# Kernel optimization log

Hardware: AMD Instinct MI355X
Metric: run time of the kernel (lower is better)

The kernel has to match this reference:

```python
import jax, jax.numpy as jnp
import numpy as np

B, IN_DIM, H1, H2, HID, SPEC_H, OUT, E = 16384, 1024, 2048, 2048, 1024, 2048, 1, 8


def setup_inputs() -> dict:
    key = jax.random.key(0)
    ks = jax.random.split(key, 12)

    def lin(k, fan_in, shape):
        # torch nn.Linear default init: U(-1/sqrt(fan_in), 1/sqrt(fan_in))
        bound = 1.0 / np.sqrt(fan_in)
        return jax.random.uniform(k, shape, jnp.float32, -bound, bound)

    return {
        "x": jax.random.normal(ks[0], (B, IN_DIM), jnp.float32),
        "d": jax.random.randint(ks[1], (B,), 0, E, jnp.int64),
        # shared encoder: Linear(IN,H1)+ReLU, Linear(H1,H2)+ReLU, Linear(H2,HID)
        "enc_W0": lin(ks[2], IN_DIM, (IN_DIM, H1)),
        "enc_b0": lin(ks[3], IN_DIM, (H1,)),
        "enc_W1": lin(ks[4], H1, (H1, H2)),
        "enc_b1": lin(ks[5], H1, (H2,)),
        "enc_W2": lin(ks[6], H2, (H2, HID)),
        "enc_b2": lin(ks[7], H2, (HID,)),
        # per-domain heads: Linear(HID,SPEC_H)+ReLU, Linear(SPEC_H,OUT)
        "spec_W1": lin(ks[8], HID, (E, HID, SPEC_H)),
        "spec_b1": lin(ks[9], HID, (E, SPEC_H)),
        "spec_W2": lin(ks[10], SPEC_H, (E, SPEC_H, OUT)),
        "spec_b2": lin(ks[11], SPEC_H, (E, OUT)),
    }


def reference(x, d, enc_W0, enc_b0, enc_W1, enc_b1, enc_W2, enc_b2,
              spec_W1, spec_b1, spec_W2, spec_b2):
    # Shared encoder (dropout is identity in eval mode)
    z = jax.nn.relu(x @ enc_W0 + enc_b0)        # [B, H1]
    z = jax.nn.relu(z @ enc_W1 + enc_b1)        # [B, H2]
    z = z @ enc_W2 + enc_b2                     # [B, HID]

    # Domain-routed heads: compute each expert on the full batch, combine by mask.
    n_experts = spec_W1.shape[0]
    out = jnp.zeros((z.shape[0], spec_W2.shape[-1]), dtype=z.dtype)  # [B, OUT]
    for e in range(n_experts):
        h = jax.nn.relu(z @ spec_W1[e] + spec_b1[e])  # [B, SPEC_H]
        y = h @ spec_W2[e] + spec_b2[e]               # [B, OUT]
        out = out + jnp.where((d == e)[:, None], y, jnp.zeros_like(y))
    return out
```

## Files before the change

### kernel.cpp

```cpp
#include <hip/hip_runtime.h>
#include <hip/hip_bf16.h>
#include <stdint.h>

#define B_SZ   16384
#define IN_DIM 1024
#define H1     2048
#define H2     2048
#define HID    1024
#define SPEC_H 2048
#define NE     8
#define MAX_TILES 136

typedef __bf16 bf16x8 __attribute__((ext_vector_type(8)));
typedef float  f32x4  __attribute__((ext_vector_type(4)));
typedef ushort us8    __attribute__((ext_vector_type(8)));

__device__ __forceinline__ ushort f2bf(float f) {
  uint32_t u = __float_as_uint(f);
  u += 0x7FFF + ((u >> 16) & 1);
  return (ushort)(u >> 16);
}

__device__ __forceinline__ void gl_lds16(const void* g, void* l) {
  __builtin_amdgcn_global_load_lds(
      (const __attribute__((address_space(1))) void*)g,
      (__attribute__((address_space(3))) void*)l, 16, 0, 0);
}


struct TransDesc { const float* src; ushort* dst; int K, N, nx, base; };

struct PrepArgs {
  TransDesc td[4];
  const float* x; ushort* xb;
  const int* d; int* counts; const float* sb2; float* out;
  int castBase;
  int cntBase;
};

__global__ void prep_all(PrepArgs pa) {
  int g = blockIdx.x;
  int t = threadIdx.x;
  if (g >= pa.cntBase) {
    __shared__ int hist[NE];
    if (t < NE) hist[t] = 0;
    __syncthreads();
    int i = (g - pa.cntBase) * 256 + t;
    int e = pa.d[i];
    atomicAdd(&hist[e], 1);
    pa.out[i] = pa.sb2[e];
    __syncthreads();
    if (t < NE) atomicAdd(&pa.counts[t], hist[t]);
    return;
  }
  if (g >= pa.castBase) {
    size_t i = (size_t)(g - pa.castBase) * 4096 + (size_t)t * 16;
    float4 v0 = *(const float4*)(pa.x + i);
    float4 v1 = *(const float4*)(pa.x + i + 4);
    float4 v2 = *(const float4*)(pa.x + i + 8);
    float4 v3 = *(const float4*)(pa.x + i + 12);
    uint32_t p0 = f2bf(v0.x) | ((uint32_t)f2bf(v0.y) << 16);
    uint32_t p1 = f2bf(v0.z) | ((uint32_t)f2bf(v0.w) << 16);
    uint32_t p2 = f2bf(v1.x) | ((uint32_t)f2bf(v1.y) << 16);
    uint32_t p3 = f2bf(v1.z) | ((uint32_t)f2bf(v1.w) << 16);
    uint32_t p4 = f2bf(v2.x) | ((uint32_t)f2bf(v2.y) << 16);
    uint32_t p5 = f2bf(v2.z) | ((uint32_t)f2bf(v2.w) << 16);
    uint32_t p6 = f2bf(v3.x) | ((uint32_t)f2bf(v3.y) << 16);
    uint32_t p7 = f2bf(v3.z) | ((uint32_t)f2bf(v3.w) << 16);
    int4 pkA = {(int)p0, (int)p1, (int)p2, (int)p3};
    int4 pkB = {(int)p4, (int)p5, (int)p6, (int)p7};
    *(int4*)(pa.xb + i) = pkA;
    *(int4*)(pa.xb + i + 8) = pkB;
    return;
  }
  __shared__ float tile[64][65];
  int wsel = 0;
#pragma unroll
  for (int i = 1; i < 4; ++i)
    if (g >= pa.td[i].base) wsel = i;
  TransDesc dd = pa.td[wsel];
  int local = g - dd.base;
  int per = dd.nx * (dd.K >> 6);
  int z = local / per;
  int r = local - z * per;
  int bx = r % dd.nx, by = r / dd.nx;
  int n0 = bx * 64, k0 = by * 64;
  const float* src = dd.src + (size_t)z * dd.K * dd.N;
  ushort* dst = dd.dst + (size_t)z * dd.K * dd.N;
  int lk = t >> 4;
  int ln4 = (t & 15) * 4;
#pragma unroll
  for (int j = 0; j < 4; ++j) {
    int k = lk + j * 16;
    float4 v = *(const float4*)(src + (size_t)(k0 + k) * dd.N + n0 + ln4);
    tile[ln4 + 0][k] = v.x;
    tile[ln4 + 1][k] = v.y;
    tile[ln4 + 2][k] = v.z;
    tile[ln4 + 3][k] = v.w;
  }
  __syncthreads();
  int kc = (t & 7) * 8;
  int nb = t >> 3;
#pragma unroll
  for (int j = 0; j < 2; ++j) {
    int nn = nb + j * 32;
    us8 o;
#pragma unroll
    for (int q = 0; q < 8; ++q) o[q] = f2bf(tile[nn][kc + q]);
    *(us8*)(dst + (size_t)(n0 + nn) * dd.K + k0 + kc) = o;
  }
}


__global__ void build_k(const int* __restrict__ counts, int* __restrict__ catalog,
                        int* __restrict__ poff, int* __restrict__ cursors) {
  if (threadIdx.x == 0) {
    int off = 0;
    for (int e = 0; e < NE; ++e) {
      poff[e] = off * 128;
      int nt = (counts[e] + 127) >> 7;
      for (int i = 0; i < nt; ++i) catalog[off + i] = e;
      off += nt;
      cursors[e] = 0;
    }
    for (int i = off; i < MAX_TILES; ++i) catalog[i] = -1;
  }
}

__global__ void scatter_k(const int* __restrict__ d, const int* __restrict__ poff,
                          int* __restrict__ cursors, int* __restrict__ perm) {
  __shared__ int wcnt[4][NE];
  __shared__ int basee[NE];
  int t = threadIdx.x;
  int i = blockIdx.x * 256 + t;
  int e = d[i];
  int w = t >> 6, lane = t & 63;
  uint64_t mymask = 0;
#pragma unroll
  for (int ee = 0; ee < NE; ++ee) {
    uint64_t mm = __ballot(e == ee);
    if (lane == 0) wcnt[w][ee] = __popcll(mm);
    if (e == ee) mymask = mm;
  }
  int rank = __popcll(mymask & ((1ull << lane) - 1ull));
  __syncthreads();
  if (t < NE) {
    int s = 0;
#pragma unroll
    for (int ww = 0; ww < 4; ++ww) { int c = wcnt[ww][t]; wcnt[ww][t] = s; s += c; }
    basee[t] = atomicAdd(&cursors[t], s);
  }
  __syncthreads();
  int pos = basee[e] + wcnt[w][e] + rank;
  perm[poff[e] + pos] = i;
}


template <int RELU>
__global__ __launch_bounds__(256, 2) void gemm_bias(
    const ushort* __restrict__ A, const ushort* __restrict__ Bt,
    const float* __restrict__ bias, ushort* __restrict__ C,
    int M, int N, int K, int lognx) {
  __shared__ __align__(16) ushort lA[128 * 64];
  __shared__ __align__(16) ushort lB[128 * 64];
  const int t = threadIdx.x;
  const int h = blockIdx.x;
  const int g = h >> 3;
  const int nx = 1 << lognx;
  const int by = (h & 7) + ((g >> lognx) << 3);
  const int bx = g & (nx - 1);
  const int m0 = by * 128, n0 = bx * 128;
  const int w = t >> 6, lane = t & 63;
  const int wm = (w >> 1) * 64, wn = (w & 1) * 64;
  const int q = lane >> 4, rl = lane & 15;

  f32x4 acc[4][4];
#pragma unroll
  for (int mi = 0; mi < 4; ++mi)
#pragma unroll
    for (int ni = 0; ni < 4; ++ni) acc[mi][ni] = 0.0f;

  const int row_s = t >> 3;
  const int pch_s = t & 7;

  for (int k0 = 0; k0 < K; k0 += 64) {
    __syncthreads();
#pragma unroll
    for (int j = 0; j < 4; ++j) {
      int row = j * 32 + row_s;
      int gch = pch_s ^ (row & 7);
      gl_lds16(A + (size_t)(m0 + row) * K + k0 + gch * 8, lA + j * 2048 + w * 512);
      gl_lds16(Bt + (size_t)(n0 + row) * K + k0 + gch * 8, lB + j * 2048 + w * 512);
    }
    __syncthreads();
#pragma unroll
    for (int kk = 0; kk < 2; ++kk) {
      bf16x8 af[4], bfr[4];
#pragma unroll
      for (int i = 0; i < 4; ++i) {
        int pc = (kk * 4 + q) ^ (rl & 7);
        af[i]  = __builtin_bit_cast(bf16x8, *(const int4*)(lA + (wm + i * 16 + rl) * 64 + pc * 8));
        bfr[i] = __builtin_bit_cast(bf16x8, *(const int4*)(lB + (wn + i * 16 + rl) * 64 + pc * 8));
      }
#pragma unroll
      for (int mi = 0; mi < 4; ++mi)
#pragma unroll
        for (int ni = 0; ni < 4; ++ni)
          acc[mi][ni] = __builtin_amdgcn_mfma_f32_16x16x32_bf16(af[mi], bfr[ni], acc[mi][ni], 0, 0, 0);
    }
  }

  float bv[4];
#pragma unroll
  for (int ni = 0; ni < 4; ++ni) bv[ni] = bias[n0 + wn + ni * 16 + rl];
#pragma unroll
  for (int mi = 0; mi < 4; ++mi) {
    int rg = m0 + wm + mi * 16 + q * 4;
#pragma unroll
    for (int r = 0; r < 4; ++r) {
#pragma unroll
      for (int ni = 0; ni < 4; ++ni) {
        float v = acc[mi][ni][r] + bv[ni];
        if (RELU) v = fmaxf(v, 0.0f);
        C[(size_t)(rg + r) * N + n0 + wn + ni * 16 + rl] = f2bf(v);
      }
    }
  }
}


template <int RELU>
__global__ __launch_bounds__(256, 2) void gemm_bias_256(
    const ushort* __restrict__ A, const ushort* __restrict__ Bt,
    const float* __restrict__ bias, ushort* __restrict__ C,
    int M, int N, int K, int lognx) {
  __shared__ __align__(16) ushort lA[256 * 64];
  __shared__ __align__(16) ushort lB[128 * 64];
  const int t = threadIdx.x;
  const int h = blockIdx.x;
  const int g = h >> 3;
  const int nx = 1 << lognx;
  const int by = (h & 7) + ((g >> lognx) << 3);
  const int bx = g & (nx - 1);
  const int m0 = by * 256, n0 = bx * 128;
  const int w = t >> 6, lane = t & 63;
  const int wm = (w >> 1) * 128, wn = (w & 1) * 64;
  const int q = lane >> 4, rl = lane & 15;

  f32x4 acc[8][4];
#pragma unroll
  for (int mi = 0; mi < 8; ++mi)
#pragma unroll
    for (int ni = 0; ni < 4; ++ni) acc[mi][ni] = 0.0f;

  const int row_s = t >> 3;
  const int pch_s = t & 7;

  for (int k0 = 0; k0 < K; k0 += 64) {
    __syncthreads();
#pragma unroll
    for (int j = 0; j < 8; ++j) {
      int row = j * 32 + row_s;
      int gch = pch_s ^ (row & 7);
      gl_lds16(A + (size_t)(m0 + row) * K + k0 + gch * 8, lA + j * 2048 + w * 512);
    }
#pragma unroll
    for (int j = 0; j < 4; ++j) {
      int row = j * 32 + row_s;
      int gch = pch_s ^ (row & 7);
      gl_lds16(Bt + (size_t)(n0 + row) * K + k0 + gch * 8, lB + j * 2048 + w * 512);
    }
    __syncthreads();
#pragma unroll
    for (int kk = 0; kk < 2; ++kk) {
      bf16x8 bfr[4];
#pragma unroll
      for (int i = 0; i < 4; ++i) {
        int pc = (kk * 4 + q) ^ (rl & 7);
        bfr[i] = __builtin_bit_cast(bf16x8, *(const int4*)(lB + (wn + i * 16 + rl) * 64 + pc * 8));
      }
#pragma unroll
      for (int mi = 0; mi < 8; ++mi) {
        int pc = (kk * 4 + q) ^ (rl & 7);
        bf16x8 af = __builtin_bit_cast(bf16x8, *(const int4*)(lA + (wm + mi * 16 + rl) * 64 + pc * 8));
#pragma unroll
        for (int ni = 0; ni < 4; ++ni)
          acc[mi][ni] = __builtin_amdgcn_mfma_f32_16x16x32_bf16(af, bfr[ni], acc[mi][ni], 0, 0, 0);
      }
    }
  }

  float bv[4];
#pragma unroll
  for (int ni = 0; ni < 4; ++ni) bv[ni] = bias[n0 + wn + ni * 16 + rl];
#pragma unroll
  for (int mi = 0; mi < 8; ++mi) {
    int rg = m0 + wm + mi * 16 + q * 4;
#pragma unroll
    for (int r = 0; r < 4; ++r) {
#pragma unroll
      for (int ni = 0; ni < 4; ++ni) {
        float v = acc[mi][ni][r] + bv[ni];
        if (RELU) v = fmaxf(v, 0.0f);
        C[(size_t)(rg + r) * N + n0 + wn + ni * 16 + rl] = f2bf(v);
      }
    }
  }
}


__global__ __launch_bounds__(256, 2) void expert_fused(
    const ushort* __restrict__ Z, const ushort* __restrict__ W1t,
    const float* __restrict__ b1, const float* __restrict__ w2,
    const int* __restrict__ perm, const int* __restrict__ catalog,
    const int* __restrict__ poff, const int* __restrict__ counts,
    float* __restrict__ out) {
  const int id = blockIdx.x;
  const int tile = (id & 7) * 17 + ((id >> 3) >> 4);
  const int ycol = (id >> 3) & 15;
  int e = catalog[tile];
  if (e < 0) return;
  __shared__ __align__(16) ushort lA[128 * 64];
  __shared__ __align__(16) ushort lB[128 * 64];
  __shared__ int perml[128];
  __shared__ float ysum[128];
  const int t = threadIdx.x;
  if (t < 128) {
    int slot = tile * 128 + t;
    int rel = slot - poff[e];
    perml[t] = (rel < counts[e]) ? perm[slot] : -1;
    ysum[t] = 0.0f;
  }
  __syncthreads();

  const int n0 = ycol * 128;
  const ushort* Bt = W1t + (size_t)e * SPEC_H * HID;
  const float* b1e = b1 + (size_t)e * SPEC_H;
  const float* w2e = w2 + (size_t)e * SPEC_H;
  const int w = t >> 6, lane = t & 63;
  const int wm = (w >> 1) * 64, wn = (w & 1) * 64;
  const int q = lane >> 4, rl = lane & 15;

  f32x4 acc[4][4];
#pragma unroll
  for (int mi = 0; mi < 4; ++mi)
#pragma unroll
    for (int ni = 0; ni < 4; ++ni) acc[mi][ni] = 0.0f;

  const int row_s = t >> 3;
  const int pch_s = t & 7;

  for (int k0 = 0; k0 < HID; k0 += 64) {
    __syncthreads();
#pragma unroll
    for (int j = 0; j < 4; ++j) {
      int row = j * 32 + row_s;
      int gch = pch_s ^ (row & 7);
      int zr = perml[row];
      zr = zr < 0 ? 0 : zr;
      gl_lds16(Z + (size_t)zr * HID + k0 + gch * 8, lA + j * 2048 + w * 512);
      gl_lds16(Bt + (size_t)(n0 + row) * HID + k0 + gch * 8, lB + j * 2048 + w * 512);
    }
    __syncthreads();
#pragma unroll
    for (int kk = 0; kk < 2; ++kk) {
      bf16x8 af[4], bfr[4];
#pragma unroll
      for (int i = 0; i < 4; ++i) {
        int pc = (kk * 4 + q) ^ (rl & 7);
        af[i]  = __builtin_bit_cast(bf16x8, *(const int4*)(lA + (wm + i * 16 + rl) * 64 + pc * 8));
        bfr[i] = __builtin_bit_cast(bf16x8, *(const int4*)(lB + (wn + i * 16 + rl) * 64 + pc * 8));
      }
#pragma unroll
      for (int mi = 0; mi < 4; ++mi)
#pragma unroll
        for (int ni = 0; ni < 4; ++ni)
          acc[mi][ni] = __builtin_amdgcn_mfma_f32_16x16x32_bf16(af[mi], bfr[ni], acc[mi][ni], 0, 0, 0);
    }
  }

  float w2v[4], b1v[4];
#pragma unroll
  for (int ni = 0; ni < 4; ++ni) {
    int n = n0 + wn + ni * 16 + rl;
    w2v[ni] = w2e[n];
    b1v[ni] = b1e[n];
  }
#pragma unroll
  for (int mi = 0; mi < 4; ++mi) {
#pragma unroll
    for (int r = 0; r < 4; ++r) {
      float p = 0.0f;
#pragma unroll
      for (int ni = 0; ni < 4; ++ni) {
        float h = acc[mi][ni][r] + b1v[ni];
        h = fmaxf(h, 0.0f);
        p += h * w2v[ni];
      }
      p += __shfl_xor(p, 1);
      p += __shfl_xor(p, 2);
      p += __shfl_xor(p, 4);
      p += __shfl_xor(p, 8);
      if (rl == 0) atomicAdd(&ysum[wm + mi * 16 + q * 4 + r], p);
    }
  }
  __syncthreads();
  if (t < 128) {
    int orow = perml[t];
    if (orow >= 0) atomicAdd(&out[orow], ysum[t]);
  }
}


extern "C" void kernel_launch(void* const* d_in, const int* in_sizes, int n_in,
                              void* d_out, int out_size, void* d_ws, size_t ws_size,
                              hipStream_t stream) {
  const float* x   = (const float*)d_in[0];
  const int*   d   = (const int*)d_in[1];
  const float* eW0 = (const float*)d_in[2];
  const float* eb0 = (const float*)d_in[3];
  const float* eW1 = (const float*)d_in[4];
  const float* eb1 = (const float*)d_in[5];
  const float* eW2 = (const float*)d_in[6];
  const float* eb2 = (const float*)d_in[7];
  const float* sW1 = (const float*)d_in[8];
  const float* sb1 = (const float*)d_in[9];
  const float* sW2 = (const float*)d_in[10];
  const float* sb2 = (const float*)d_in[11];
  float* out = (float*)d_out;

  const size_t fixed = ((size_t)(4 + 8 + 4 + 32 + 32 + 32) << 20) + (1 << 20);
  int CH = 8192;
  if (ws_size >= fixed + (size_t)16384 * 8192) CH = 16384;

  char* p = (char*)d_ws;
  ushort* W0t  = (ushort*)p; p += (size_t)IN_DIM * H1 * 2;
  ushort* W1t  = (ushort*)p; p += (size_t)H1 * H2 * 2;
  ushort* W2t  = (ushort*)p; p += (size_t)H2 * HID * 2;
  ushort* sW1t = (ushort*)p; p += (size_t)NE * HID * SPEC_H * 2;
  ushort* Zb   = (ushort*)p; p += (size_t)B_SZ * HID * 2;
  ushort* xb   = (ushort*)p; p += (size_t)B_SZ * IN_DIM * 2;
  int* counts  = (int*)p; p += 64;
  int* cursors = (int*)p; p += 64;
  int* poff    = (int*)p; p += 64;
  int* catalog = (int*)p; p += 1024;
  int* perm    = (int*)p; p += (size_t)MAX_TILES * 128 * 4;
  p = (char*)(((uintptr_t)p + 255) & ~(uintptr_t)255);
  ushort* z1 = (ushort*)p; p += (size_t)CH * H1 * 2;
  ushort* z2 = (ushort*)p; p += (size_t)CH * H2 * 2;

  hipMemsetAsync(counts, 0, 64, stream);

  PrepArgs pa;
  pa.td[0] = {eW0, W0t, IN_DIM, H1, H1 / 64, 0};
  pa.td[1] = {eW1, W1t, H1, H2, H2 / 64, 512};
  pa.td[2] = {eW2, W2t, H2, HID, HID / 64, 1536};
  pa.td[3] = {sW1, sW1t, HID, SPEC_H, SPEC_H / 64, 2048};
  pa.x = x; pa.xb = xb;
  pa.d = d; pa.counts = counts; pa.sb2 = sb2; pa.out = out;
  pa.castBase = 6144;
  pa.cntBase = 6144 + 4096;
  prep_all<<<6144 + 4096 + 64, 256, 0, stream>>>(pa);

  build_k<<<1, 64, 0, stream>>>(counts, catalog, poff, cursors);
  scatter_k<<<B_SZ / 256, 256, 0, stream>>>(d, poff, cursors, perm);

  for (int c = 0; c < B_SZ; c += CH) {
    gemm_bias<1><<<(CH / 128) * (H1 / 128), 256, 0, stream>>>(
        xb + (size_t)c * IN_DIM, W0t, eb0, z1, CH, H1, IN_DIM, 4);
    gemm_bias_256<1><<<(CH / 256) * (H2 / 128), 256, 0, stream>>>(
        z1, W1t, eb1, z2, CH, H2, H1, 4);
    gemm_bias<0><<<(CH / 128) * (HID / 128), 256, 0, stream>>>(
        z2, W2t, eb2, Zb + (size_t)c * HID, CH, HID, H2, 3);
  }

  expert_fused<<<MAX_TILES * 16, 256, 0, stream>>>(
      Zb, sW1t, sb1, sW2, perm, catalog, poff, counts, out);
}
```

Measured before the change: 538.6 us.

## Replace encoder GEMMs with 256x256 double-buffered 8-wave pipelined kernel

Replaces the two encoder GEMM kernels with one 512-thread kernel that computes a 256x256 output tile. It double-buffers LDS and interleaves the global-to-LDS loads for future K tiles with MFMA phases, using manual waitcnt, barriers and setprio. The aim is to hide memory latency and raise operand reuse per loaded byte. In exchange it uses 128KB of LDS per block, launches fewer blocks, and depends on fragile hand-written wait counts.

```diff
diff --git a/kernel.cpp b/kernel.cpp
--- a/kernel.cpp
+++ b/kernel.cpp
@@ -157,137 +157,156 @@
 
 
 template <int RELU>
-__global__ __launch_bounds__(256, 2) void gemm_bias(
+__global__ __launch_bounds__(512, 2) void gemm8(
     const ushort* __restrict__ A, const ushort* __restrict__ Bt,
     const float* __restrict__ bias, ushort* __restrict__ C,
     int M, int N, int K, int lognx) {
-  __shared__ __align__(16) ushort lA[128 * 64];
-  __shared__ __align__(16) ushort lB[128 * 64];
+  __shared__ __align__(16) ushort sm[65536];
   const int t = threadIdx.x;
   const int h = blockIdx.x;
   const int g = h >> 3;
   const int nx = 1 << lognx;
   const int by = (h & 7) + ((g >> lognx) << 3);
   const int bx = g & (nx - 1);
-  const int m0 = by * 128, n0 = bx * 128;
+  const int m0 = by * 256, n0 = bx * 256;
   const int w = t >> 6, lane = t & 63;
-  const int wm = (w >> 1) * 64, wn = (w & 1) * 64;
+  const int wm = (w >> 2) * 128, wn = (w & 3) * 64;
   const int q = lane >> 4, rl = lane & 15;
-
-  f32x4 acc[4][4];
-#pragma unroll
-  for (int mi = 0; mi < 4; ++mi)
+  const int row_s = t >> 3, pch_s = t & 7;
+  const int NT = K >> 6;
+
+  f32x4 acc[8][4];
+#pragma unroll
+  for (int mi = 0; mi < 8; ++mi)
 #pragma unroll
     for (int ni = 0; ni < 4; ++ni) acc[mi][ni] = 0.0f;
 
-  const int row_s = t >> 3;
-  const int pch_s = t & 7;
-
-  for (int k0 = 0; k0 < K; k0 += 64) {
-    __syncthreads();
-#pragma unroll
-    for (int j = 0; j < 4; ++j) {
-      int row = j * 32 + row_s;
-      int gch = pch_s ^ (row & 7);
-      gl_lds16(A + (size_t)(m0 + row) * K + k0 + gch * 8, lA + j * 2048 + w * 512);
-      gl_lds16(Bt + (size_t)(n0 + row) * K + k0 + gch * 8, lB + j * 2048 + w * 512);
-    }
-    __syncthreads();
-#pragma unroll
-    for (int kk = 0; kk < 2; ++kk) {
-      bf16x8 af[4], bfr[4];
-#pragma unroll
-      for (int i = 0; i < 4; ++i) {
-        int pc = (kk * 4 + q) ^ (rl & 7);
-        af[i]  = __builtin_bit_cast(bf16x8, *(const int4*)(lA + (wm + i * 16 + rl) * 64 + pc * 8));
-        bfr[i] = __builtin_bit_cast(bf16x8, *(const int4*)(lB + (wn + i * 16 + rl) * 64 + pc * 8));
-      }
+  bf16x8 afr[4][2], bfr[4][2];
+
+  auto STG = [&](int tt, int which) {
+    if (tt >= NT) return;
+    const int c = tt & 1;
+    const int k0 = tt << 6;
+    if (which >= 2) {
+      const int R0 = (which - 2) << 7;
+#pragma unroll
+      for (int j = 0; j < 2; ++j) {
+        int row = (j << 6) + row_s;
+        int gch = pch_s ^ (row & 7);
+        gl_lds16(A + (size_t)(m0 + R0 + row) * K + k0 + (gch << 3),
+                 sm + (c << 15) + (R0 << 6) + (j << 12) + (w << 9));
+      }
+    } else {
+      const int R0 = which << 7;
+#pragma unroll
+      for (int j = 0; j < 2; ++j) {
+        int row = (j << 6) + row_s;
+        int gch = pch_s ^ (row & 7);
+        gl_lds16(Bt + (size_t)(n0 + R0 + row) * K + k0 + (gch << 3),
+                 sm + (c << 15) + 16384 + (R0 << 6) + (j << 12) + (w << 9));
+      }
+    }
+  };
+
+  STG(0, 0); STG(0, 1); STG(0, 2); STG(0, 3);
+  asm volatile("s_waitcnt vmcnt(4)" ::: "memory");
+  STG(1, 0); STG(1, 1); STG(1, 2);
+  asm volatile("s_waitcnt vmcnt(6)" ::: "memory");
+  __builtin_amdgcn_s_barrier();
+
+  for (int tt = 0; tt < NT; ++tt) {
+    const ushort* bufA = sm + ((tt & 1) << 15);
+    const ushort* bufB = bufA + 16384;
+
+#pragma unroll
+    for (int mi = 0; mi < 4; ++mi)
+#pragma unroll
+      for (int kk = 0; kk < 2; ++kk) {
+        int pc = ((kk << 2) + q) ^ (rl & 7);
+        afr[mi][kk] = __builtin_bit_cast(bf16x8,
+            *(const int4*)(bufA + (wm + (mi << 4) + rl) * 64 + (pc << 3)));
+      }
+#pragma unroll
+    for (int ni = 0; ni < 4; ++ni)
+#pragma unroll
+      for (int kk = 0; kk < 2; ++kk) {
+        int pc = ((kk << 2) + q) ^ (rl & 7);
+        bfr[ni][kk] = __builtin_bit_cast(bf16x8,
+            *(const int4*)(bufB + (wn + (ni << 4) + rl) * 64 + (pc << 3)));
+      }
+    asm volatile("" ::: "memory");
+    __builtin_amdgcn_sched_barrier(0);
+    STG(tt + 1, 3);
+    __builtin_amdgcn_s_barrier();
+    asm volatile("s_waitcnt lgkmcnt(0)" ::: "memory");
+    __builtin_amdgcn_sched_barrier(0);
+    __builtin_amdgcn_s_setprio(1);
+#pragma unroll
+    for (int kk = 0; kk < 2; ++kk)
 #pragma unroll
       for (int mi = 0; mi < 4; ++mi)
 #pragma unroll
-        for (int ni = 0; ni < 4; ++ni)
-          acc[mi][ni] = __builtin_amdgcn_mfma_f32_16x16x32_bf16(af[mi], bfr[ni], acc[mi][ni], 0, 0, 0);
-    }
-  }
-
-  float bv[4];
-#pragma unroll
-  for (int ni = 0; ni < 4; ++ni) bv[ni] = bias[n0 + wn + ni * 16 + rl];
-#pragma unroll
-  for (int mi = 0; mi < 4; ++mi) {
-    int rg = m0 + wm + mi * 16 + q * 4;
-#pragma unroll
-    for (int r = 0; r < 4; ++r) {
-#pragma unroll
-      for (int ni = 0; ni < 4; ++ni) {
-        float v = acc[mi][ni][r] + bv[ni];
-        if (RELU) v = fmaxf(v, 0.0f);
-        C[(size_t)(rg + r) * N + n0 + wn + ni * 16 + rl] = f2bf(v);
-      }
-    }
-  }
-}
-
-
-template <int RELU>
-__global__ __launch_bounds__(256, 2) void gemm_bias_256(
-    const ushort* __restrict__ A, const ushort* __restrict__ Bt,
-    const float* __restrict__ bias, ushort* __restrict__ C,
-    int M, int N, int K, int lognx) {
-  __shared__ __align__(16) ushort lA[256 * 64];
-  __shared__ __align__(16) ushort lB[128 * 64];
-  const int t = threadIdx.x;
-  const int h = blockIdx.x;
-  const int g = h >> 3;
-  const int nx = 1 << lognx;
-  const int by = (h & 7) + ((g >> lognx) << 3);
-  const int bx = g & (nx - 1);
-  const int m0 = by * 256, n0 = bx * 128;
-  const int w = t >> 6, lane = t & 63;
-  const int wm = (w >> 1) * 128, wn = (w & 1) * 64;
-  const int q = lane >> 4, rl = lane & 15;
-
-  f32x4 acc[8][4];
-#pragma unroll
-  for (int mi = 0; mi < 8; ++mi)
-#pragma unroll
-    for (int ni = 0; ni < 4; ++ni) acc[mi][ni] = 0.0f;
-
-  const int row_s = t >> 3;
-  const int pch_s = t & 7;
-
-  for (int k0 = 0; k0 < K; k0 += 64) {
-    __syncthreads();
-#pragma unroll
-    for (int j = 0; j < 8; ++j) {
-      int row = j * 32 + row_s;
-      int gch = pch_s ^ (row & 7);
-      gl_lds16(A + (size_t)(m0 + row) * K + k0 + gch * 8, lA + j * 2048 + w * 512);
-    }
-#pragma unroll
-    for (int j = 0; j < 4; ++j) {
-      int row = j * 32 + row_s;
-      int gch = pch_s ^ (row & 7);
-      gl_lds16(Bt + (size_t)(n0 + row) * K + k0 + gch * 8, lB + j * 2048 + w * 512);
-    }
-    __syncthreads();
-#pragma unroll
-    for (int kk = 0; kk < 2; ++kk) {
-      bf16x8 bfr[4];
-#pragma unroll
-      for (int i = 0; i < 4; ++i) {
-        int pc = (kk * 4 + q) ^ (rl & 7);
-        bfr[i] = __builtin_bit_cast(bf16x8, *(const int4*)(lB + (wn + i * 16 + rl) * 64 + pc * 8));
-      }
-#pragma unroll
-      for (int mi = 0; mi < 8; ++mi) {
-        int pc = (kk * 4 + q) ^ (rl & 7);
-        bf16x8 af = __builtin_bit_cast(bf16x8, *(const int4*)(lA + (wm + mi * 16 + rl) * 64 + pc * 8));
-#pragma unroll
-        for (int ni = 0; ni < 4; ++ni)
-          acc[mi][ni] = __builtin_amdgcn_mfma_f32_16x16x32_bf16(af, bfr[ni], acc[mi][ni], 0, 0, 0);
-      }
-    }
+        for (int ni = 0; ni < 2; ++ni)
+          acc[mi][ni] = __builtin_amdgcn_mfma_f32_16x16x32_bf16(
+              afr[mi][kk], bfr[ni][kk], acc[mi][ni], 0, 0, 0);
+    __builtin_amdgcn_s_setprio(0);
+    __builtin_amdgcn_s_barrier();
+
+    STG(tt + 2, 0);
+    __builtin_amdgcn_s_barrier();
+    __builtin_amdgcn_s_setprio(1);
+#pragma unroll
+    for (int kk = 0; kk < 2; ++kk)
+#pragma unroll
+      for (int mi = 0; mi < 4; ++mi)
+#pragma unroll
+        for (int ni = 2; ni < 4; ++ni)
+          acc[mi][ni] = __builtin_amdgcn_mfma_f32_16x16x32_bf16(
+              afr[mi][kk], bfr[ni][kk], acc[mi][ni], 0, 0, 0);
+    __builtin_amdgcn_s_setprio(0);
+    __builtin_amdgcn_s_barrier();
+
+#pragma unroll
+    for (int mi = 0; mi < 4; ++mi)
+#pragma unroll
+      for (int kk = 0; kk < 2; ++kk) {
+        int pc = ((kk << 2) + q) ^ (rl & 7);
+        afr[mi][kk] = __builtin_bit_cast(bf16x8,
+            *(const int4*)(bufA + (wm + ((mi + 4) << 4) + rl) * 64 + (pc << 3)));
+      }
+    asm volatile("" ::: "memory");
+    __builtin_amdgcn_sched_barrier(0);
+    STG(tt + 2, 1);
+    __builtin_amdgcn_s_barrier();
+    asm volatile("s_waitcnt lgkmcnt(0)" ::: "memory");
+    __builtin_amdgcn_sched_barrier(0);
+    __builtin_amdgcn_s_setprio(1);
+#pragma unroll
+    for (int kk = 0; kk < 2; ++kk)
+#pragma unroll
+      for (int mi = 0; mi < 4; ++mi)
+#pragma unroll
+        for (int ni = 0; ni < 2; ++ni)
+          acc[mi + 4][ni] = __builtin_amdgcn_mfma_f32_16x16x32_bf16(
+              afr[mi][kk], bfr[ni][kk], acc[mi + 4][ni], 0, 0, 0);
+    __builtin_amdgcn_s_setprio(0);
+    __builtin_amdgcn_s_barrier();
+
+    STG(tt + 2, 2);
+    if (tt + 2 < NT)      asm volatile("s_waitcnt vmcnt(6)" ::: "memory");
+    else if (tt + 1 < NT) asm volatile("s_waitcnt vmcnt(0)" ::: "memory");
+    __builtin_amdgcn_s_barrier();
+    __builtin_amdgcn_s_setprio(1);
+#pragma unroll
+    for (int kk = 0; kk < 2; ++kk)
+#pragma unroll
+      for (int mi = 0; mi < 4; ++mi)
+#pragma unroll
+        for (int ni = 2; ni < 4; ++ni)
+          acc[mi + 4][ni] = __builtin_amdgcn_mfma_f32_16x16x32_bf16(
+              afr[mi][kk], bfr[ni][kk], acc[mi + 4][ni], 0, 0, 0);
+    __builtin_amdgcn_s_setprio(0);
+    __builtin_amdgcn_s_barrier();
   }
 
   float bv[4];
@@ -466,12 +485,12 @@
   scatter_k<<<B_SZ / 256, 256, 0, stream>>>(d, poff, cursors, perm);
 
   for (int c = 0; c < B_SZ; c += CH) {
-    gemm_bias<1><<<(CH / 128) * (H1 / 128), 256, 0, stream>>>(
-        xb + (size_t)c * IN_DIM, W0t, eb0, z1, CH, H1, IN_DIM, 4);
-    gemm_bias_256<1><<<(CH / 256) * (H2 / 128), 256, 0, stream>>>(
-        z1, W1t, eb1, z2, CH, H2, H1, 4);
-    gemm_bias<0><<<(CH / 128) * (HID / 128), 256, 0, stream>>>(
-        z2, W2t, eb2, Zb + (size_t)c * HID, CH, HID, H2, 3);
+    gemm8<1><<<(CH / 256) * (H1 / 256), 512, 0, stream>>>(
+        xb + (size_t)c * IN_DIM, W0t, eb0, z1, CH, H1, IN_DIM, 3);
+    gemm8<1><<<(CH / 256) * (H2 / 256), 512, 0, stream>>>(
+        z1, W1t, eb1, z2, CH, H2, H1, 3);
+    gemm8<0><<<(CH / 256) * (HID / 256), 512, 0, stream>>>(
+        z2, W2t, eb2, Zb + (size_t)c * HID, CH, HID, H2, 2);
   }
 
   expert_fused<<<MAX_TILES * 16, 256, 0, stream>>>(
```

New measurement: 570.1 us. +5.8%, slower.

## Use 256-row tiles for encoder GEMMs and expert kernel; split middle GEMM

Applied to the files above, without the earlier changes.

Switches the first and last encoder GEMMs from 128x128 tiles to the 256x128 kernel, and enlarges the expert_fused kernel to 256-row tiles with 8x4 accumulators per wave, regrouping experts into 256-row tiles. The middle GEMM is split into two half-batch launches. Larger M tiles raise reuse of each weight tile and cut the number of blocks and loads. In exchange they use more registers, and expert padding waste grows with 256-row granularity. The W2 GEMM now uses nx=8 with 256-row tiles, which changes the grid swizzle.

```diff
diff --git a/kernel.cpp b/kernel.cpp
--- a/kernel.cpp
+++ b/kernel.cpp
@@ -9,7 +9,7 @@
 #define HID    1024
 #define SPEC_H 2048
 #define NE     8
-#define MAX_TILES 136
+#define ETILES 72
 
 typedef __bf16 bf16x8 __attribute__((ext_vector_type(8)));
 typedef float  f32x4  __attribute__((ext_vector_type(4)));
@@ -117,13 +117,13 @@
   if (threadIdx.x == 0) {
     int off = 0;
     for (int e = 0; e < NE; ++e) {
-      poff[e] = off * 128;
-      int nt = (counts[e] + 127) >> 7;
+      poff[e] = off * 256;
+      int nt = (counts[e] + 255) >> 8;
       for (int i = 0; i < nt; ++i) catalog[off + i] = e;
       off += nt;
       cursors[e] = 0;
     }
-    for (int i = off; i < MAX_TILES; ++i) catalog[i] = -1;
+    for (int i = off; i < ETILES; ++i) catalog[i] = -1;
   }
 }
 
@@ -153,79 +153,6 @@
   __syncthreads();
   int pos = basee[e] + wcnt[w][e] + rank;
   perm[poff[e] + pos] = i;
-}
-
-
-template <int RELU>
-__global__ __launch_bounds__(256, 2) void gemm_bias(
-    const ushort* __restrict__ A, const ushort* __restrict__ Bt,
-    const float* __restrict__ bias, ushort* __restrict__ C,
-    int M, int N, int K, int lognx) {
-  __shared__ __align__(16) ushort lA[128 * 64];
-  __shared__ __align__(16) ushort lB[128 * 64];
-  const int t = threadIdx.x;
-  const int h = blockIdx.x;
-  const int g = h >> 3;
-  const int nx = 1 << lognx;
-  const int by = (h & 7) + ((g >> lognx) << 3);
-  const int bx = g & (nx - 1);
-  const int m0 = by * 128, n0 = bx * 128;
-  const int w = t >> 6, lane = t & 63;
-  const int wm = (w >> 1) * 64, wn = (w & 1) * 64;
-  const int q = lane >> 4, rl = lane & 15;
-
-  f32x4 acc[4][4];
-#pragma unroll
-  for (int mi = 0; mi < 4; ++mi)
-#pragma unroll
-    for (int ni = 0; ni < 4; ++ni) acc[mi][ni] = 0.0f;
-
-  const int row_s = t >> 3;
-  const int pch_s = t & 7;
-
-  for (int k0 = 0; k0 < K; k0 += 64) {
-    __syncthreads();
-#pragma unroll
-    for (int j = 0; j < 4; ++j) {
-      int row = j * 32 + row_s;
-      int gch = pch_s ^ (row & 7);
-      gl_lds16(A + (size_t)(m0 + row) * K + k0 + gch * 8, lA + j * 2048 + w * 512);
-      gl_lds16(Bt + (size_t)(n0 + row) * K + k0 + gch * 8, lB + j * 2048 + w * 512);
-    }
-    __syncthreads();
-#pragma unroll
-    for (int kk = 0; kk < 2; ++kk) {
-      bf16x8 af[4], bfr[4];
-#pragma unroll
-      for (int i = 0; i < 4; ++i) {
-        int pc = (kk * 4 + q) ^ (rl & 7);
-        af[i]  = __builtin_bit_cast(bf16x8, *(const int4*)(lA + (wm + i * 16 + rl) * 64 + pc * 8));
-        bfr[i] = __builtin_bit_cast(bf16x8, *(const int4*)(lB + (wn + i * 16 + rl) * 64 + pc * 8));
-      }
-#pragma unroll
-      for (int mi = 0; mi < 4; ++mi)
-#pragma unroll
-        for (int ni = 0; ni < 4; ++ni)
-          acc[mi][ni] = __builtin_amdgcn_mfma_f32_16x16x32_bf16(af[mi], bfr[ni], acc[mi][ni], 0, 0, 0);
-    }
-  }
-
-  float bv[4];
-#pragma unroll
-  for (int ni = 0; ni < 4; ++ni) bv[ni] = bias[n0 + wn + ni * 16 + rl];
-#pragma unroll
-  for (int mi = 0; mi < 4; ++mi) {
-    int rg = m0 + wm + mi * 16 + q * 4;
-#pragma unroll
-    for (int r = 0; r < 4; ++r) {
-#pragma unroll
-      for (int ni = 0; ni < 4; ++ni) {
-        float v = acc[mi][ni][r] + bv[ni];
-        if (RELU) v = fmaxf(v, 0.0f);
-        C[(size_t)(rg + r) * N + n0 + wn + ni * 16 + rl] = f2bf(v);
-      }
-    }
-  }
 }
 
 
@@ -316,17 +243,17 @@
     const int* __restrict__ poff, const int* __restrict__ counts,
     float* __restrict__ out) {
   const int id = blockIdx.x;
-  const int tile = (id & 7) * 17 + ((id >> 3) >> 4);
+  const int tile = (id & 7) * 9 + ((id >> 3) >> 4);
   const int ycol = (id >> 3) & 15;
   int e = catalog[tile];
   if (e < 0) return;
-  __shared__ __align__(16) ushort lA[128 * 64];
+  __shared__ __align__(16) ushort lA[256 * 64];
   __shared__ __align__(16) ushort lB[128 * 64];
-  __shared__ int perml[128];
-  __shared__ float ysum[128];
+  __shared__ int perml[256];
+  __shared__ float ysum[256];
   const int t = threadIdx.x;
-  if (t < 128) {
-    int slot = tile * 128 + t;
+  {
+    int slot = tile * 256 + t;
     int rel = slot - poff[e];
     perml[t] = (rel < counts[e]) ? perm[slot] : -1;
     ysum[t] = 0.0f;
@@ -338,12 +265,12 @@
   const float* b1e = b1 + (size_t)e * SPEC_H;
   const float* w2e = w2 + (size_t)e * SPEC_H;
   const int w = t >> 6, lane = t & 63;
-  const int wm = (w >> 1) * 64, wn = (w & 1) * 64;
+  const int wm = (w >> 1) * 128, wn = (w & 1) * 64;
   const int q = lane >> 4, rl = lane & 15;
 
-  f32x4 acc[4][4];
-#pragma unroll
-  for (int mi = 0; mi < 4; ++mi)
+  f32x4 acc[8][4];
+#pragma unroll
+  for (int mi = 0; mi < 8; ++mi)
 #pragma unroll
     for (int ni = 0; ni < 4; ++ni) acc[mi][ni] = 0.0f;
 
@@ -353,29 +280,36 @@
   for (int k0 = 0; k0 < HID; k0 += 64) {
     __syncthreads();
 #pragma unroll
-    for (int j = 0; j < 4; ++j) {
+    for (int j = 0; j < 8; ++j) {
       int row = j * 32 + row_s;
       int gch = pch_s ^ (row & 7);
       int zr = perml[row];
       zr = zr < 0 ? 0 : zr;
       gl_lds16(Z + (size_t)zr * HID + k0 + gch * 8, lA + j * 2048 + w * 512);
+    }
+#pragma unroll
+    for (int j = 0; j < 4; ++j) {
+      int row = j * 32 + row_s;
+      int gch = pch_s ^ (row & 7);
       gl_lds16(Bt + (size_t)(n0 + row) * HID + k0 + gch * 8, lB + j * 2048 + w * 512);
     }
     __syncthreads();
 #pragma unroll
     for (int kk = 0; kk < 2; ++kk) {
-      bf16x8 af[4], bfr[4];
+      bf16x8 bfr[4];
 #pragma unroll
       for (int i = 0; i < 4; ++i) {
         int pc = (kk * 4 + q) ^ (rl & 7);
-        af[i]  = __builtin_bit_cast(bf16x8, *(const int4*)(lA + (wm + i * 16 + rl) * 64 + pc * 8));
         bfr[i] = __builtin_bit_cast(bf16x8, *(const int4*)(lB + (wn + i * 16 + rl) * 64 + pc * 8));
       }
 #pragma unroll
-      for (int mi = 0; mi < 4; ++mi)
+      for (int mi = 0; mi < 8; ++mi) {
+        int pc = (kk * 4 + q) ^ (rl & 7);
+        bf16x8 af = __builtin_bit_cast(bf16x8, *(const int4*)(lA + (wm + mi * 16 + rl) * 64 + pc * 8));
 #pragma unroll
         for (int ni = 0; ni < 4; ++ni)
-          acc[mi][ni] = __builtin_amdgcn_mfma_f32_16x16x32_bf16(af[mi], bfr[ni], acc[mi][ni], 0, 0, 0);
+          acc[mi][ni] = __builtin_amdgcn_mfma_f32_16x16x32_bf16(af, bfr[ni], acc[mi][ni], 0, 0, 0);
+      }
     }
   }
 
@@ -387,7 +321,7 @@
     b1v[ni] = b1e[n];
   }
 #pragma unroll
-  for (int mi = 0; mi < 4; ++mi) {
+  for (int mi = 0; mi < 8; ++mi) {
 #pragma unroll
     for (int r = 0; r < 4; ++r) {
       float p = 0.0f;
@@ -405,7 +339,7 @@
     }
   }
   __syncthreads();
-  if (t < 128) {
+  {
     int orow = perml[t];
     if (orow >= 0) atomicAdd(&out[orow], ysum[t]);
   }
@@ -444,7 +378,7 @@
   int* cursors = (int*)p; p += 64;
   int* poff    = (int*)p; p += 64;
   int* catalog = (int*)p; p += 1024;
-  int* perm    = (int*)p; p += (size_t)MAX_TILES * 128 * 4;
+  int* perm    = (int*)p; p += (size_t)ETILES * 256 * 4;
   p = (char*)(((uintptr_t)p + 255) & ~(uintptr_t)255);
   ushort* z1 = (ushort*)p; p += (size_t)CH * H1 * 2;
   ushort* z2 = (ushort*)p; p += (size_t)CH * H2 * 2;
@@ -466,14 +400,17 @@
   scatter_k<<<B_SZ / 256, 256, 0, stream>>>(d, poff, cursors, perm);
 
   for (int c = 0; c < B_SZ; c += CH) {
-    gemm_bias<1><<<(CH / 128) * (H1 / 128), 256, 0, stream>>>(
+    gemm_bias_256<1><<<(CH / 256) * (H1 / 128), 256, 0, stream>>>(
         xb + (size_t)c * IN_DIM, W0t, eb0, z1, CH, H1, IN_DIM, 4);
-    gemm_bias_256<1><<<(CH / 256) * (H2 / 128), 256, 0, stream>>>(
-        z1, W1t, eb1, z2, CH, H2, H1, 4);
-    gemm_bias<0><<<(CH / 128) * (HID / 128), 256, 0, stream>>>(
+    const int HM = CH / 2;
+    gemm_bias_256<1><<<(HM / 256) * (H2 / 128), 256, 0, stream>>>(
+        z1, W1t, eb1, z2, HM, H2, H1, 4);
+    gemm_bias_256<1><<<(HM / 256) * (H2 / 128), 256, 0, stream>>>(
+        z1 + (size_t)HM * H1, W1t, eb1, z2 + (size_t)HM * H2, HM, H2, H1, 4);
+    gemm_bias_256<0><<<(CH / 256) * (HID / 128), 256, 0, stream>>>(
         z2, W2t, eb2, Zb + (size_t)c * HID, CH, HID, H2, 3);
   }
 
-  expert_fused<<<MAX_TILES * 16, 256, 0, stream>>>(
+  expert_fused<<<ETILES * 16, 256, 0, stream>>>(
       Zb, sW1t, sb1, sW2, perm, catalog, poff, counts, out);
 }
```

After: 564.6 us. 4.8% more time.
